# Performance work log

Hardware: AMD Instinct MI355X
Metric: run time of the kernel (lower is better)

The kernel has to match this reference:

```python
import jax, jax.numpy as jnp
import numpy as np

INV_L_MIN, INV_L_MAX = 0.5, 2.0

def _gelu(v):
    return jax.nn.gelu(v, approximate=False)  # torch F.gelu default = exact erf

def compute_gradient(f, directed_edges, edge_gradient_weights):
    # f: [b, c, n] ; directed_edges: [b, e, 2] (target, source) ; egw: [b, e, d]
    f = jnp.transpose(f, (0, 2, 1))                      # [b, n, c]
    b, n, c = f.shape
    e, d = edge_gradient_weights.shape[1], edge_gradient_weights.shape[2]
    target, source = directed_edges[..., 0], directed_edges[..., 1]
    fs = jnp.take_along_axis(f, source[:, :, None], axis=1)   # [b, e, c]
    ft = jnp.take_along_axis(f, target[:, :, None], axis=1)   # [b, e, c]
    # einsum('bed,bec->becd') then reshape -> channel-major (c*d) layout
    msg = (edge_gradient_weights[:, :, None, :] * (fs - ft)[:, :, :, None]).reshape(b, e, c * d)
    seg = (target + n * jnp.arange(b, dtype=target.dtype)[:, None]).reshape(-1)
    grad = jax.ops.segment_sum(msg.reshape(b * e, c * d), seg, num_segments=b * n)
    return jnp.transpose(grad.reshape(b, n, c * d), (0, 2, 1))  # [b, c*d, n]

def spectral_conv(x, wc, ws_, w0, bc, bs, b0, wbc, wbs, wb0):
    # x: [b, c, n]; bases: [b, n, k, w]; weights: [c, o, k, w]
    xc = jnp.einsum('bcx,bxkw->bckw', x, wbc)
    xs = jnp.einsum('bcx,bxkw->bckw', x, wbs)
    x0 = jnp.einsum('bcx,bxkw->bckw', x, wb0)
    fc = jnp.einsum('bckw,cokw->bokw', xc, wc) - jnp.einsum('bckw,cokw->bokw', xs, ws_)
    fs = jnp.einsum('bckw,cokw->bokw', xs, wc) + jnp.einsum('bckw,cokw->bokw', xc, ws_)
    f0 = jnp.einsum('bckw,cokw->bokw', x0, w0)
    return (jnp.einsum('bokw,bxkw->box', f0, b0)
            + 2 * jnp.einsum('bokw,bxkw->box', fc, bc)
            - 2 * jnp.einsum('bokw,bxkw->box', fs, bs))

def setup_inputs():
    key = jax.random.key(0)
    ks = jax.random.split(key, 16)
    B, N, E = 4, 20000, 100000
    NDIMS, NMEAS, NMODES = 3, 1, 32
    C, L = 128, 3
    IN_DIM, FC_DIM, OUT_DIM = 3, 128, 1
    f32 = jnp.float32
    inp = {}
    inp['x'] = jax.random.normal(ks[0], (B, N, IN_DIM), f32)
    inp['node_mask'] = jnp.ones((B, N, 1), jnp.int32)
    inp['nodes'] = jax.random.uniform(ks[1], (B, N, NDIMS), f32)
    inp['node_weights'] = jax.random.uniform(ks[2], (B, N, NMEAS), f32) / N
    inp['directed_edges'] = jax.random.randint(ks[3], (B, E, 2), 0, N, jnp.int32)
    inp['edge_gradient_weights'] = jax.random.normal(ks[4], (B, E, NDIMS), f32)
    # modes k = 2*pi*K/L0, K integer-like
    inp['modes'] = (2 * jnp.pi * jax.random.randint(ks[5], (NMODES, NDIMS, NMEAS), 1, 9)).astype(f32)
    # scaled_logit(1.0, 0.5, 2.0): sigmoid(l)=1/3 -> l=log(0.5)
    inp['inv_L_scale_latent'] = jnp.full((NDIMS, NMEAS), np.log(0.5), f32)
    inp['fc0_w'] = jax.random.normal(ks[6], (C, IN_DIM), f32) / np.sqrt(IN_DIM)
    inp['fc0_b'] = jnp.zeros((C,), f32)
    sc = 1.0 / (C * C)
    inp['swc'] = sc * jax.random.uniform(ks[7], (L, C, C, NMODES, NMEAS), f32)
    inp['sws'] = sc * jax.random.uniform(ks[8], (L, C, C, NMODES, NMEAS), f32)
    inp['sw0'] = sc * jax.random.uniform(ks[9], (L, C, C, 1, NMEAS), f32)
    inp['ww'] = jax.random.normal(ks[10], (L, C, C), f32) / np.sqrt(C)
    inp['wb'] = jnp.zeros((L, C), f32)
    inp['gw'] = jax.random.normal(ks[11], (L, C, NDIMS * C), f32) / np.sqrt(NDIMS * C)
    inp['gb'] = jnp.zeros((L, C), f32)
    inp['fc1_w'] = jax.random.normal(ks[12], (FC_DIM, C), f32) / np.sqrt(C)
    inp['fc1_b'] = jnp.zeros((FC_DIM,), f32)
    inp['fc2_w'] = jax.random.normal(ks[13], (OUT_DIM, FC_DIM), f32) / np.sqrt(FC_DIM)
    inp['fc2_b'] = jnp.zeros((OUT_DIM,), f32)
    return inp

def reference(x, node_mask, nodes, node_weights, directed_edges, edge_gradient_weights,
              modes, inv_L_scale_latent, fc0_w, fc0_b, swc, sws, sw0, ww, wb, gw, gb,
              fc1_w, fc1_b, fc2_w, fc2_b):
    inv_L = INV_L_MIN + (INV_L_MAX - INV_L_MIN) * jax.nn.sigmoid(inv_L_scale_latent)  # [d, w]
    t = jnp.einsum('bxd,kdw->bxkw', nodes, modes * inv_L[None])
    bc, bs = jnp.cos(t), jnp.sin(t)
    b0 = jnp.ones(t.shape[:2] + (1, t.shape[3]), t.dtype)
    w = node_weights[:, :, None, :]
    wbc, wbs, wb0 = bc * w, bs * w, b0 * w
    h = jnp.einsum('bni,ci->bnc', x, fc0_w) + fc0_b        # lift
    h = jnp.transpose(h, (0, 2, 1))                        # [b, C, n]
    L = swc.shape[0]
    for i in range(L):
        h1 = spectral_conv(h, swc[i], sws[i], sw0[i], bc, bs, b0, wbc, wbs, wb0)
        h2 = jnp.einsum('oc,bcn->bon', ww[i], h) + wb[i][None, :, None]
        g = compute_gradient(h, directed_edges, edge_gradient_weights)
        h3 = jnp.einsum('oc,bcn->bon', gw[i], g) + gb[i][None, :, None]
        h = h1 + h2 + h3
        if i != L - 1:
            h = _gelu(h)
    h = jnp.transpose(h, (0, 2, 1))                        # [b, n, C]
    h = _gelu(h @ fc1_w.T + fc1_b)
    return h @ fc2_w.T + fc2_b                             # [b, n, out_dim]
```

## Files before the change

kernel.cpp:

```cpp
#include <hip/hip_runtime.h>
#include <math.h>

#define B_ 4
#define N_ 20000
#define E_ 100000
#define C_ 128
#define K_ 32
#define NPAD 20480
#define NROWS (B_*N_ + 128)

typedef __attribute__((ext_vector_type(8))) short short8;
typedef __attribute__((ext_vector_type(4))) float floatx4;
typedef __attribute__((ext_vector_type(4))) unsigned int uintx4;
typedef __attribute__((ext_vector_type(2))) unsigned int uintx2;

__device__ __forceinline__ float gelu_exact(float x){
    return 0.5f * x * (1.0f + erff(x * 0.70710678118654752f));
}

__device__ __forceinline__ unsigned short f2bf(float f){
    unsigned int u = __builtin_bit_cast(unsigned int, f);
    u += 0x7FFFu + ((u >> 16) & 1u);
    return (unsigned short)(u >> 16);
}
__device__ __forceinline__ unsigned int pack2(float a, float b){
    return (unsigned int)f2bf(a) | ((unsigned int)f2bf(b) << 16);
}
__device__ __forceinline__ float bf2f(unsigned short u){
    unsigned int v = ((unsigned int)u) << 16;
    return __builtin_bit_cast(float, v);
}
__device__ __forceinline__ float u2f(unsigned int u){
    return __builtin_bit_cast(float, u);
}


__global__ __launch_bounds__(256) void basis_kernel(
    const float* __restrict__ nodes, const float* __restrict__ nw,
    const float* __restrict__ modes, const float* __restrict__ latent,
    unsigned short* __restrict__ bcb, unsigned short* __restrict__ bsb,
    unsigned short* __restrict__ wBt)
{
    __shared__ float lx[64], ly[64], lz[64], lwv[64];
    __shared__ unsigned short lTc[32*64], lTs[32*64];
    int b = blockIdx.y, n0 = blockIdx.x*64;
    int tid = threadIdx.x;
    size_t bN = (size_t)b*N_;
    if (tid < 64){
        int n = n0 + tid;
        float iL0 = 0.5f + 1.5f/(1.f+expf(-latent[0]));
        float iL1 = 0.5f + 1.5f/(1.f+expf(-latent[1]));
        float iL2 = 0.5f + 1.5f/(1.f+expf(-latent[2]));
        if (n < N_){
            lx[tid] = nodes[(bN+n)*3+0]*iL0;
            ly[tid] = nodes[(bN+n)*3+1]*iL1;
            lz[tid] = nodes[(bN+n)*3+2]*iL2;
            lwv[tid] = nw[bN+n];
        } else { lx[tid]=0.f; ly[tid]=0.f; lz[tid]=0.f; lwv[tid]=0.f; }
    }
    __syncthreads();
    int node = tid>>2, k0 = (tid&3)*8;
    float p0 = lx[node], p1 = ly[node], p2 = lz[node], w = lwv[node];
    float cv[8], sv[8];
    #pragma unroll
    for (int i=0;i<8;i++){
        int k = k0+i;
        float t = p0*modes[k*3+0] + p1*modes[k*3+1] + p2*modes[k*3+2];
        cv[i] = cosf(t); sv[i] = sinf(t);
        lTc[k*64 + node] = f2bf(w*cv[i]);
        lTs[k*64 + node] = f2bf(w*sv[i]);
    }
    int gn = n0 + node;
    if (gn < N_){
        uintx4 uc = (uintx4){pack2(cv[0],cv[1]), pack2(cv[2],cv[3]),
                             pack2(cv[4],cv[5]), pack2(cv[6],cv[7])};
        uintx4 us = (uintx4){pack2(sv[0],sv[1]), pack2(sv[2],sv[3]),
                             pack2(sv[4],sv[5]), pack2(sv[6],sv[7])};
        *(uintx4*)&bcb[(bN+gn)*K_ + k0] = uc;
        *(uintx4*)&bsb[(bN+gn)*K_ + k0] = us;
    }
    __syncthreads();
    #pragma unroll
    for (int i=0;i<5;i++){
        int idx = i*256 + tid;
        int row = idx>>4, seg = idx&15;
        unsigned short v0,v1,v2,v3;
        if (row < 32){
            v0=lTc[row*64+seg*4+0]; v1=lTc[row*64+seg*4+1];
            v2=lTc[row*64+seg*4+2]; v3=lTc[row*64+seg*4+3];
        } else if (row < 64){
            int r = row-32;
            v0=lTs[r*64+seg*4+0]; v1=lTs[r*64+seg*4+1];
            v2=lTs[r*64+seg*4+2]; v3=lTs[r*64+seg*4+3];
        } else if (row == 64){
            v0=f2bf(lwv[seg*4+0]); v1=f2bf(lwv[seg*4+1]);
            v2=f2bf(lwv[seg*4+2]); v3=f2bf(lwv[seg*4+3]);
        } else { v0=v1=v2=v3=0; }
        uintx2 u;
        u.x = (unsigned int)v0 | ((unsigned int)v1<<16);
        u.y = (unsigned int)v2 | ((unsigned int)v3<<16);
        *(uintx2*)&wBt[((size_t)b*80+row)*NPAD + n0 + seg*4] = u;
    }
}


__global__ __launch_bounds__(256) void fc0_kernel(
    const float* __restrict__ x, const float* __restrict__ w,
    const float* __restrict__ bvec, unsigned short* __restrict__ hN,
    unsigned short* __restrict__ hT)
{
    int idx = blockIdx.x*256 + threadIdx.x;
    if (idx >= B_*N_) return;
    int b = idx / N_, n = idx - b*N_;
    float x0 = x[(size_t)idx*3+0], x1 = x[(size_t)idx*3+1], x2 = x[(size_t)idx*3+2];
    unsigned short* hr = hN + (size_t)idx*C_;
    for (int c=0;c<C_;c+=4){
        float4 v;
        v.x = bvec[c+0] + x0*w[(c+0)*3] + x1*w[(c+0)*3+1] + x2*w[(c+0)*3+2];
        v.y = bvec[c+1] + x0*w[(c+1)*3] + x1*w[(c+1)*3+1] + x2*w[(c+1)*3+2];
        v.z = bvec[c+2] + x0*w[(c+2)*3] + x1*w[(c+2)*3+1] + x2*w[(c+2)*3+2];
        v.w = bvec[c+3] + x0*w[(c+3)*3] + x1*w[(c+3)*3+1] + x2*w[(c+3)*3+2];
        uintx2 u; u.x = pack2(v.x,v.y); u.y = pack2(v.z,v.w);
        *(uintx2*)(hr+c) = u;
        hT[((size_t)b*C_+c+0)*NPAD + n] = f2bf(v.x);
        hT[((size_t)b*C_+c+1)*NPAD + n] = f2bf(v.y);
        hT[((size_t)b*C_+c+2)*NPAD + n] = f2bf(v.z);
        hT[((size_t)b*C_+c+3)*NPAD + n] = f2bf(v.w);
    }
}


__global__ __launch_bounds__(256) void hist_kernel(
    const int* __restrict__ edges, int* __restrict__ cnt)
{
    int idx = blockIdx.x*256 + threadIdx.x;
    if (idx >= B_*E_) return;
    int b = idx / E_;
    int t = edges[(size_t)idx*2];
    atomicAdd(cnt + b*N_ + t, 1);
}

__global__ __launch_bounds__(1024) void scan_kernel(
    const int* __restrict__ cnt, int* __restrict__ rowptr, int* __restrict__ cur)
{
    __shared__ int wsum[16];
    int b = blockIdx.x, tid = threadIdx.x;
    int lane = tid & 63, wv = tid >> 6;
    const int CHUNK = 20;
    int start = tid * CHUNK;
    int lc[CHUNK];
    int lsum = 0;
    #pragma unroll
    for (int i=0;i<CHUNK;i++){
        int n = start + i;
        int v = (n < N_) ? cnt[b*N_+n] : 0;
        lc[i] = v; lsum += v;
    }
    int v = lsum;
    #pragma unroll
    for (int off=1; off<64; off<<=1){
        int t = __shfl_up(v, off, 64);
        if (lane >= off) v += t;
    }
    if (lane == 63) wsum[wv] = v;
    __syncthreads();
    if (wv == 0 && lane < 16){
        int wv2 = wsum[lane];
        #pragma unroll
        for (int off=1; off<16; off<<=1){
            int t = __shfl_up(wv2, off, 64);
            if (lane >= off) wv2 += t;
        }
        wsum[lane] = wv2;
    }
    __syncthreads();
    int waveoff = (wv == 0) ? 0 : wsum[wv-1];
    int excl = waveoff + v - lsum;
    #pragma unroll
    for (int i=0;i<CHUNK;i++){
        int n = start + i;
        if (n < N_){
            rowptr[b*(N_+1)+n] = excl;
            cur[b*N_+n] = excl;
            excl += lc[i];
        }
    }
    if (tid == 0) rowptr[b*(N_+1)+N_] = E_;
}

__global__ __launch_bounds__(256) void fill_kernel(
    const int* __restrict__ edges, const float* __restrict__ egw,
    int* __restrict__ cur, uintx4* __restrict__ epack)
{
    int idx = blockIdx.x*256 + threadIdx.x;
    if (idx >= B_*E_) return;
    int b = idx / E_;
    int t = edges[(size_t)idx*2];
    int src = edges[(size_t)idx*2+1];
    uintx4 rec;
    rec.x = (unsigned int)src;
    rec.y = __builtin_bit_cast(unsigned int, egw[(size_t)idx*3+0]);
    rec.z = __builtin_bit_cast(unsigned int, egw[(size_t)idx*3+1]);
    rec.w = __builtin_bit_cast(unsigned int, egw[(size_t)idx*3+2]);
    int pos = atomicAdd(cur + b*N_ + t, 1);
    epack[(size_t)b*E_ + pos] = rec;
}


__global__ __launch_bounds__(256) void wconv_kernel(
    const float* __restrict__ ww, const float* __restrict__ gw,
    unsigned short* __restrict__ wcat3)
{
    int o = blockIdx.x, l = blockIdx.y, t = threadIdx.x;
    const float* ww_l = ww + (size_t)l*C_*C_;
    const float* gw_l = gw + (size_t)l*C_*C_*3;
    int k = t*2;
    float a, bv;
    if (k < 128){ a = ww_l[(size_t)o*C_ + k];      bv = ww_l[(size_t)o*C_ + k + 1]; }
    else        { a = gw_l[(size_t)o*384 + k-128]; bv = gw_l[(size_t)o*384 + k-127]; }
    *(unsigned int*)&wcat3[((size_t)l*C_ + o)*512 + k] = pack2(a, bv);
}

__global__ __launch_bounds__(64) void fc1conv_kernel(
    const float* __restrict__ fc1w, unsigned short* __restrict__ w16)
{
    int o = blockIdx.x, t = threadIdx.x;
    int k = t*2;
    *(unsigned int*)&w16[(size_t)o*C_ + k] = pack2(fc1w[(size_t)o*C_+k], fc1w[(size_t)o*C_+k+1]);
}


__global__ __launch_bounds__(256) void stageA_kernel(
    const unsigned short* __restrict__ hT, const unsigned short* __restrict__ wBt,
    float* __restrict__ part)
{
    __shared__ unsigned short As[80*72];
    __shared__ unsigned short Bs[128*72];
    int b = blockIdx.y, blk = blockIdx.x;
    int tid = threadIdx.x;
    int wv = tid>>6, lane = tid&63, l15 = lane&15, quad = lane>>4;
    floatx4 acc[5][2];
    #pragma unroll
    for (int mt=0;mt<5;mt++){ acc[mt][0]=(floatx4){0,0,0,0}; acc[mt][1]=(floatx4){0,0,0,0}; }
    size_t hbase = (size_t)b*C_*NPAD;
    size_t wbase = (size_t)b*80*NPAD;
    for (int cidx=0; cidx<5; ++cidx){
        int n0c = blk*320 + cidx*64;
        #pragma unroll
        for (int i=0;i<3;i++){
            int idx = i*256 + tid;
            if (idx < 640){
                int row = idx>>3, seg = idx&7;
                uintx4 v = *(const uintx4*)&wBt[wbase + (size_t)row*NPAD + n0c + seg*8];
                *(uintx4*)&As[row*72 + seg*8] = v;
            }
        }
        #pragma unroll
        for (int i=0;i<4;i++){
            int idx = i*256 + tid;
            int row = idx>>3, seg = idx&7;
            int node = n0c + seg*8;
            uintx4 v = (uintx4){0,0,0,0};
            if (node < N_)
                v = *(const uintx4*)&hT[hbase + (size_t)row*NPAD + node];
            *(uintx4*)&Bs[row*72 + seg*8] = v;
        }
        __syncthreads();
        #pragma unroll
        for (int ks=0; ks<2; ks++){
            short8 bfrag[2];
            #pragma unroll
            for (int ot=0;ot<2;ot++)
                bfrag[ot] = *(const short8*)&Bs[(wv*32+ot*16+l15)*72 + ks*32 + quad*8];
            #pragma unroll
            for (int mt=0;mt<5;mt++){
                short8 af = *(const short8*)&As[(mt*16+l15)*72 + ks*32 + quad*8];
                acc[mt][0] = __builtin_amdgcn_mfma_f32_16x16x32_bf16(af, bfrag[0], acc[mt][0], 0,0,0);
                acc[mt][1] = __builtin_amdgcn_mfma_f32_16x16x32_bf16(af, bfrag[1], acc[mt][1], 0,0,0);
            }
        }
        __syncthreads();
    }
    float* pblk = part + ((size_t)(b*64+blk))*80*C_;
    #pragma unroll
    for (int mt=0;mt<5;mt++){
        #pragma unroll
        for (int ot=0;ot<2;ot++){
            int c = wv*32 + ot*16 + l15;
            #pragma unroll
            for (int r=0;r<4;r++){
                int kcol = mt*16 + quad*4 + r;
                pblk[kcol*C_ + c] = acc[mt][ot][r];
            }
        }
    }
}

__global__ __launch_bounds__(256) void reducePart_kernel(
    const float* __restrict__ part, float* __restrict__ xq)
{
    int idx = blockIdx.x*256 + threadIdx.x;
    if (idx >= B_*80*C_) return;
    int b = idx / (80*C_);
    int r = idx - b*80*C_;
    float s = 0.f;
    for (int blk=0; blk<64; blk++)
        s += part[((size_t)(b*64+blk))*80*C_ + r];
    xq[idx] = s;
}


__global__ __launch_bounds__(256) void mix_kernel(
    const float* __restrict__ xq, const float* __restrict__ swc_l,
    const float* __restrict__ sws_l, const float* __restrict__ sw0_l,
    unsigned short* __restrict__ wfb, float* __restrict__ f0)
{
    __shared__ float s64[4][64];
    int o = blockIdx.x, tid = threadIdx.x;
    int b = tid >> 6, t = tid & 63;
    int k = t & 31; bool isS = t >= 32;
    const float* xqb = xq + (size_t)b*80*C_;
    float acc = 0.f;
    for (int c=0;c<C_;c++){
        float xc = xqb[k*C_ + c], xs = xqb[(32+k)*C_ + c];
        float wc = swc_l[((size_t)c*C_+o)*K_ + k];
        float ws = sws_l[((size_t)c*C_+o)*K_ + k];
        acc += isS ? (xs*wc + xc*ws) : (xc*wc - xs*ws);
    }
    wfb[((size_t)b*C_+o)*64 + t] = f2bf(isS ? -2.f*acc : 2.f*acc);
    float p = xqb[64*C_ + t]      * sw0_l[(size_t)t*C_+o]
            + xqb[64*C_ + 64 + t] * sw0_l[(size_t)(t+64)*C_+o];
    s64[b][t] = p; __syncthreads();
    if (t==0){
        float s=0.f;
        for (int i=0;i<64;i++) s += s64[b][i];
        f0[b*C_+o] = s;
    }
}


__global__ __launch_bounds__(256) void grad_kernel(
    const unsigned short* __restrict__ hN, const uintx4* __restrict__ epack,
    const int* __restrict__ rowptr, unsigned short* __restrict__ g)
{
    int flat = blockIdx.x;
    int xcd = flat & 7;
    int b = xcd >> 1;
    int grp = (flat >> 3)*2 + (xcd & 1);
    int n = grp*4 + (threadIdx.x >> 6);
    int cp = threadIdx.x & 63;
    size_t bN = (size_t)b*N_;
    size_t bE = (size_t)b*E_;
    int r0 = rowptr[b*(N_+1)+n], r1 = rowptr[b*(N_+1)+n+1];
    unsigned int hcu = *(const unsigned int*)&hN[(bN+n)*C_ + cp*2];
    float hc0 = bf2f((unsigned short)hcu), hc1 = bf2f((unsigned short)(hcu>>16));
    float a00=0.f,a01=0.f,a02=0.f, a10=0.f,a11=0.f,a12=0.f;
    int i = r0;
    for (; i + 1 < r1; i += 2){
        uintx4 p0 = epack[bE + i];
        uintx4 p1 = epack[bE + i + 1];
        int s0 = (int)p0.x, s1 = (int)p1.x;
        unsigned int u0 = *(const unsigned int*)&hN[(bN+s0)*C_ + cp*2];
        unsigned int u1 = *(const unsigned int*)&hN[(bN+s1)*C_ + cp*2];
        float w00 = u2f(p0.y), w01 = u2f(p0.z), w02 = u2f(p0.w);
        float w10 = u2f(p1.y), w11 = u2f(p1.z), w12 = u2f(p1.w);
        float d00 = bf2f((unsigned short)u0) - hc0;
        float d01 = bf2f((unsigned short)(u0>>16)) - hc1;
        float d10 = bf2f((unsigned short)u1) - hc0;
        float d11 = bf2f((unsigned short)(u1>>16)) - hc1;
        a00 += w00*d00; a01 += w01*d00; a02 += w02*d00;
        a10 += w00*d01; a11 += w01*d01; a12 += w02*d01;
        a00 += w10*d10; a01 += w11*d10; a02 += w12*d10;
        a10 += w10*d11; a11 += w11*d11; a12 += w12*d11;
    }
    if (i < r1){
        uintx4 p0 = epack[bE + i];
        int s0 = (int)p0.x;
        unsigned int u0 = *(const unsigned int*)&hN[(bN+s0)*C_ + cp*2];
        float w00 = u2f(p0.y), w01 = u2f(p0.z), w02 = u2f(p0.w);
        float d00 = bf2f((unsigned short)u0) - hc0;
        float d01 = bf2f((unsigned short)(u0>>16)) - hc1;
        a00 += w00*d00; a01 += w01*d00; a02 += w02*d00;
        a10 += w00*d01; a11 += w01*d01; a12 += w02*d01;
    }
    unsigned short* gr = g + (bN+n)*(size_t)384 + cp*6;
    *(unsigned int*)(gr+0) = pack2(a00,a01);
    *(unsigned int*)(gr+2) = pack2(a02,a10);
    *(unsigned int*)(gr+4) = pack2(a11,a12);
}


__global__ __launch_bounds__(256) void gemm_kernel(
    const unsigned short* __restrict__ hN, const unsigned short* __restrict__ g,
    const unsigned short* __restrict__ bcb, const unsigned short* __restrict__ bsb,
    const unsigned short* __restrict__ wcat, const unsigned short* __restrict__ wfb,
    const float* __restrict__ wb_l, const float* __restrict__ gb_l,
    const float* __restrict__ f0,
    unsigned short* __restrict__ hNo, unsigned short* __restrict__ hT, int apply_gelu)
{
    __shared__ unsigned short As[2][64*72];
    int b = blockIdx.y;
    int nb0 = blockIdx.x*64;
    int tid = threadIdx.x;
    int a_n = tid>>2, a_s = tid&3;
    int wv = tid>>6, lane = tid&63, l15 = lane&15, quad = lane>>4;
    floatx4 acc[4][2];
    #pragma unroll
    for (int mt=0;mt<4;mt++)
        #pragma unroll
        for (int ot=0;ot<2;ot++) acc[mt][ot] = (floatx4){0.f,0.f,0.f,0.f};
    size_t bN = (size_t)b*N_;
    int gn = nb0 + a_n; bool av = gn < N_;
    size_t row = bN + (size_t)(av ? gn : 0);
    const unsigned short* hrow  = hN + row*C_;
    const unsigned short* grow  = g  + row*384;
    const unsigned short* bcrow = bcb + row*K_;
    const unsigned short* bsrow = bsb + row*K_;
    int o0 = wv*32 + l15, o1 = o0 + 16;
    const unsigned short* w0p = wcat + (size_t)o0*512 + quad*8;
    const unsigned short* w1p = wcat + (size_t)o1*512 + quad*8;
    const unsigned short* fb0 = wfb + ((size_t)b*C_ + o0)*64 + quad*8;
    const unsigned short* fb1 = wfb + ((size_t)b*C_ + o1)*64 + quad*8;

    auto loadA = [&](int ch, uintx4& v0, uintx4& v1){
        v0 = (uintx4){0,0,0,0}; v1 = (uintx4){0,0,0,0};
        if (av){
            if (ch < 8){
                const uintx4* p = (ch<2) ? (const uintx4*)(hrow + ch*64 + a_s*16)
                                         : (const uintx4*)(grow + (ch-2)*64 + a_s*16);
                v0 = p[0]; v1 = p[1];
            } else {
                const uintx4* p = (a_s < 2) ? (const uintx4*)(bcrow + a_s*16)
                                            : (const uintx4*)(bsrow + (a_s-2)*16);
                v0 = p[0]; v1 = p[1];
            }
        }
    };

    uintx4 c0, c1;
    loadA(0, c0, c1);
    *(uintx4*)&As[0][a_n*72 + a_s*16]     = c0;
    *(uintx4*)&As[0][a_n*72 + a_s*16 + 8] = c1;
    int p = 0;
    for (int ch=0; ch<9; ++ch){
        uintx4 n0v, n1v;
        if (ch < 8) loadA(ch+1, n0v, n1v);
        __syncthreads();
        #pragma unroll
        for (int ks=0; ks<2; ks++){
            short8 bfr0, bfr1;
            if (ch < 8){
                bfr0 = *(const short8*)(w0p + ch*64 + ks*32);
                bfr1 = *(const short8*)(w1p + ch*64 + ks*32);
            } else {
                bfr0 = *(const short8*)(fb0 + ks*32);
                bfr1 = *(const short8*)(fb1 + ks*32);
            }
            #pragma unroll
            for (int mt=0; mt<4; mt++){
                short8 af = *(const short8*)&As[p][(mt*16+l15)*72 + ks*32 + quad*8];
                acc[mt][0] = __builtin_amdgcn_mfma_f32_16x16x32_bf16(af, bfr0, acc[mt][0], 0,0,0);
                acc[mt][1] = __builtin_amdgcn_mfma_f32_16x16x32_bf16(af, bfr1, acc[mt][1], 0,0,0);
            }
        }
        if (ch < 8){
            *(uintx4*)&As[1-p][a_n*72 + a_s*16]     = n0v;
            *(uintx4*)&As[1-p][a_n*72 + a_s*16 + 8] = n1v;
            p ^= 1;
        }
    }
    float biasv[2]; int oo[2];
    oo[0]=o0; oo[1]=o1;
    #pragma unroll
    for (int ot=0;ot<2;ot++)
        biasv[ot] = wb_l[oo[ot]] + gb_l[oo[ot]] + f0[(size_t)b*C_ + oo[ot]];
    unsigned short* AsF = &As[0][0];
    if (apply_gelu) __syncthreads();
    #pragma unroll
    for (int mt=0;mt<4;mt++){
        #pragma unroll
        for (int ot=0;ot<2;ot++){
            int nb = nb0 + mt*16 + quad*4;
            float v4[4];
            #pragma unroll
            for (int r=0;r<4;r++){
                float vv = acc[mt][ot][r] + biasv[ot];
                if (apply_gelu) vv = gelu_exact(vv);
                v4[r] = vv;
                if (nb + r < N_) hNo[(bN+nb+r)*C_ + oo[ot]] = f2bf(vv);
            }
            if (apply_gelu){
                uintx2 u; u.x = pack2(v4[0],v4[1]); u.y = pack2(v4[2],v4[3]);
                *(uintx2*)&AsF[oo[ot]*72 + mt*16 + quad*4] = u;
            }
        }
    }
    if (apply_gelu){
        __syncthreads();
        int orow = tid>>1, half = tid&1;
        uintx4 u0 = *(const uintx4*)&AsF[orow*72 + half*32];
        uintx4 u1 = *(const uintx4*)&AsF[orow*72 + half*32 + 8];
        unsigned short* dst = &hT[((size_t)b*C_ + orow)*NPAD + nb0 + half*32];
        *(uintx4*)dst       = u0;
        *(uintx4*)(dst + 8) = u1;
    }
}


__global__ __launch_bounds__(256) void final_kernel(
    const unsigned short* __restrict__ hN, const unsigned short* __restrict__ fc1b16,
    const float* __restrict__ fc1b, const float* __restrict__ fc2w,
    const float* __restrict__ fc2b, float* __restrict__ out)
{
    __shared__ unsigned short As[64*72];
    __shared__ float pp[4*64];
    int b = blockIdx.y;
    int nb0 = blockIdx.x*64;
    int tid = threadIdx.x;
    int a_n = tid>>2, a_s = tid&3;
    int wv = tid>>6, lane = tid&63, l15 = lane&15, quad = lane>>4;
    floatx4 acc[4][2];
    #pragma unroll
    for (int mt=0;mt<4;mt++){ acc[mt][0]=(floatx4){0,0,0,0}; acc[mt][1]=(floatx4){0,0,0,0}; }
    size_t bN = (size_t)b*N_;
    int gn = nb0 + a_n; bool av = gn < N_;
    size_t row = bN + (size_t)(av ? gn : 0);
    const unsigned short* hrow = hN + row*C_;
    int o0 = wv*32 + l15, o1 = o0 + 16;
    const unsigned short* w0p = fc1b16 + (size_t)o0*C_ + quad*8;
    const unsigned short* w1p = fc1b16 + (size_t)o1*C_ + quad*8;

    for (int ch=0; ch<2; ++ch){
        uintx4 v0 = (uintx4){0,0,0,0}, v1 = (uintx4){0,0,0,0};
        if (av){
            const uintx4* pptr = (const uintx4*)(hrow + ch*64 + a_s*16);
            v0 = pptr[0]; v1 = pptr[1];
        }
        *(uintx4*)&As[a_n*72 + a_s*16]     = v0;
        *(uintx4*)&As[a_n*72 + a_s*16 + 8] = v1;
        __syncthreads();
        #pragma unroll
        for (int ks=0; ks<2; ks++){
            short8 bfr0 = *(const short8*)(w0p + ch*64 + ks*32);
            short8 bfr1 = *(const short8*)(w1p + ch*64 + ks*32);
            #pragma unroll
            for (int mt=0; mt<4; mt++){
                short8 af = *(const short8*)&As[(mt*16+l15)*72 + ks*32 + quad*8];
                acc[mt][0] = __builtin_amdgcn_mfma_f32_16x16x32_bf16(af, bfr0, acc[mt][0], 0,0,0);
                acc[mt][1] = __builtin_amdgcn_mfma_f32_16x16x32_bf16(af, bfr1, acc[mt][1], 0,0,0);
            }
        }
        __syncthreads();
    }
    float fw0 = fc2w[o0], fw1 = fc2w[o1];
    float b0 = fc1b[o0], b1 = fc1b[o1];
    #pragma unroll
    for (int mt=0;mt<4;mt++){
        float s[4];
        #pragma unroll
        for (int r=0;r<4;r++)
            s[r] = fw0*gelu_exact(acc[mt][0][r] + b0) + fw1*gelu_exact(acc[mt][1][r] + b1);
        #pragma unroll
        for (int m=1;m<16;m<<=1)
            #pragma unroll
            for (int r=0;r<4;r++)
                s[r] += __shfl_xor(s[r], m, 16);
        if (l15 < 4){
            float v = (l15==0)?s[0]:(l15==1)?s[1]:(l15==2)?s[2]:s[3];
            pp[wv*64 + mt*16 + quad*4 + l15] = v;
        }
    }
    __syncthreads();
    if (tid < 64){
        float sum = pp[tid] + pp[64+tid] + pp[128+tid] + pp[192+tid] + fc2b[0];
        int n = nb0 + tid;
        if (n < N_) out[bN + n] = sum;
    }
}


extern "C" void kernel_launch(void* const* d_in, const int* in_sizes, int n_in,
                              void* d_out, int out_size, void* d_ws, size_t ws_size,
                              hipStream_t stream)
{
    const float* x      = (const float*)d_in[0];
    const float* nodes  = (const float*)d_in[2];
    const float* nw     = (const float*)d_in[3];
    const int*   edges  = (const int*)  d_in[4];
    const float* egw    = (const float*)d_in[5];
    const float* modes  = (const float*)d_in[6];
    const float* latent = (const float*)d_in[7];
    const float* fc0w   = (const float*)d_in[8];
    const float* fc0b   = (const float*)d_in[9];
    const float* swc    = (const float*)d_in[10];
    const float* sws    = (const float*)d_in[11];
    const float* sw0    = (const float*)d_in[12];
    const float* ww     = (const float*)d_in[13];
    const float* wb     = (const float*)d_in[14];
    const float* gw     = (const float*)d_in[15];
    const float* gb     = (const float*)d_in[16];
    const float* fc1w   = (const float*)d_in[17];
    const float* fc1b   = (const float*)d_in[18];
    const float* fc2w   = (const float*)d_in[19];
    const float* fc2b   = (const float*)d_in[20];
    float* out = (float*)d_out;

    char* W = (char*)d_ws;
    size_t off = 0;
    unsigned short* bcB = (unsigned short*)(W+off); off += (size_t)NROWS*K_*2;
    unsigned short* bsB = (unsigned short*)(W+off); off += (size_t)NROWS*K_*2;
    unsigned short* wBt = (unsigned short*)(W+off); off += (size_t)B_*80*NPAD*2;
    unsigned short* hT  = (unsigned short*)(W+off); off += (size_t)B_*C_*NPAD*2;
    unsigned short* hNa = (unsigned short*)(W+off); off += (size_t)NROWS*C_*2;
    unsigned short* hNb = (unsigned short*)(W+off); off += (size_t)NROWS*C_*2;
    unsigned short* g   = (unsigned short*)(W+off); off += (size_t)NROWS*C_*3*2;
    unsigned short* wcat3=(unsigned short*)(W+off); off += (size_t)3*C_*512*2;
    unsigned short* wfb = (unsigned short*)(W+off); off += (size_t)B_*C_*64*2;
    unsigned short* fcw16=(unsigned short*)(W+off); off += (size_t)C_*C_*2;
    float* part = (float*)(W+off); off += (size_t)B_*64*80*C_*4;
    float* xq   = (float*)(W+off); off += (size_t)B_*80*C_*4;
    float* f0   = (float*)(W+off); off += (size_t)B_*C_*4;
    off = (off + 15) & ~(size_t)15;
    uintx4* epack = (uintx4*)(W+off); off += (size_t)B_*E_*16;
    int* cnt    = (int*)(W+off); off += (size_t)B_*N_*4;
    int* rowptr = (int*)(W+off); off += (size_t)B_*(N_+1)*4 + 16;
    int* cur    = (int*)(W+off); off += (size_t)B_*N_*4;

    (void)hipMemsetAsync(cnt, 0, (size_t)B_*N_*sizeof(int), stream);
    basis_kernel<<<dim3(NPAD/64, B_), 256, 0, stream>>>(
        nodes, nw, modes, latent, bcB, bsB, wBt);
    fc0_kernel  <<<(B_*N_+255)/256, 256, 0, stream>>>(x, fc0w, fc0b, hNa, hT);
    hist_kernel <<<(B_*E_+255)/256, 256, 0, stream>>>(edges, cnt);
    scan_kernel <<<B_, 1024, 0, stream>>>(cnt, rowptr, cur);
    fill_kernel <<<(B_*E_+255)/256, 256, 0, stream>>>(edges, egw, cur, epack);
    wconv_kernel<<<dim3(C_,3), 256, 0, stream>>>(ww, gw, wcat3);
    fc1conv_kernel<<<C_, 64, 0, stream>>>(fc1w, fcw16);

    unsigned short* hc = hNa; unsigned short* hn = hNb;
    for (int l=0; l<3; ++l){
        stageA_kernel<<<dim3(64,B_), 256, 0, stream>>>(hT, wBt, part);
        reducePart_kernel<<<(B_*80*C_+255)/256, 256, 0, stream>>>(part, xq);
        mix_kernel<<<C_, 256, 0, stream>>>(
            xq, swc + (size_t)l*C_*C_*K_, sws + (size_t)l*C_*C_*K_,
            sw0 + (size_t)l*C_*C_, wfb, f0);
        grad_kernel<<<N_, 256, 0, stream>>>(hc, epack, rowptr, g);
        gemm_kernel<<<dim3((N_+63)/64,B_), 256, 0, stream>>>(
            hc, g, bcB, bsB, wcat3 + (size_t)l*C_*512, wfb,
            wb + (size_t)l*C_, gb + (size_t)l*C_,
            f0, hn, hT, (l<2) ? 1 : 0);
        unsigned short* t = hc; hc = hn; hn = t;
    }
    final_kernel<<<dim3((N_+63)/64,B_), 256, 0, stream>>>(
        hc, fcw16, fc1b, fc2w, fc2b, out);
}
```

Before: 569.7 us.

## Pipeline GEMM A-tiles via direct global-to-LDS loads with a four-stage ring

In gemm_kernel, the register-staged, double-buffered shared-memory load of the A operand is replaced by asynchronous global_load_lds transfers into a four-slot LDS ring. The tile layout changes from padded rows to an XOR-swizzled layout so fragment reads avoid bank conflicts. Weight B fragments are preloaded into a three-deep register ring, and hand-placed vmcnt waits plus barriers order the stages. The aim is to hide global-load latency behind MFMA work and drop the VGPR round-trip for A. In exchange, the per-row bounds check is gone, so the last block reads past N into adjacent or padded rows, and the hand-counted waits are fragile.

```diff
diff --git a/kernel.cpp b/kernel.cpp
--- a/kernel.cpp
+++ b/kernel.cpp
@@ -390,6 +390,9 @@
 }
 
 
+#define WAITV(n) asm volatile("s_waitcnt vmcnt(" #n ")" ::: "memory")
+#define BAR() __builtin_amdgcn_s_barrier()
+
 __global__ __launch_bounds__(256) void gemm_kernel(
     const unsigned short* __restrict__ hN, const unsigned short* __restrict__ g,
     const unsigned short* __restrict__ bcb, const unsigned short* __restrict__ bsb,
@@ -398,11 +401,10 @@
     const float* __restrict__ f0,
     unsigned short* __restrict__ hNo, unsigned short* __restrict__ hT, int apply_gelu)
 {
-    __shared__ unsigned short As[2][64*72];
+    __shared__ unsigned short As4[4][4096];
     int b = blockIdx.y;
     int nb0 = blockIdx.x*64;
     int tid = threadIdx.x;
-    int a_n = tid>>2, a_s = tid&3;
     int wv = tid>>6, lane = tid&63, l15 = lane&15, quad = lane>>4;
     floatx4 acc[4][2];
     #pragma unroll
@@ -410,71 +412,80 @@
         #pragma unroll
         for (int ot=0;ot<2;ot++) acc[mt][ot] = (floatx4){0.f,0.f,0.f,0.f};
     size_t bN = (size_t)b*N_;
-    int gn = nb0 + a_n; bool av = gn < N_;
-    size_t row = bN + (size_t)(av ? gn : 0);
-    const unsigned short* hrow  = hN + row*C_;
-    const unsigned short* grow  = g  + row*384;
-    const unsigned short* bcrow = bcb + row*K_;
-    const unsigned short* bsrow = bsb + row*K_;
+
+    const unsigned short* sh[2]; const unsigned short* sg[2]; const unsigned short* sb[2];
+    #pragma unroll
+    for (int q=0;q<2;q++){
+        int li = q*256 + tid;
+        int row = li>>3, col = (li&7) ^ (row&7);
+        size_t gr = bN + (size_t)(nb0 + row);
+        sh[q] = hN + gr*C_  + col*8;
+        sg[q] = g  + gr*384 + col*8;
+        sb[q] = (col < 4) ? (bcb + gr*K_ + col*8) : (bsb + gr*K_ + (col-4)*8);
+    }
     int o0 = wv*32 + l15, o1 = o0 + 16;
     const unsigned short* w0p = wcat + (size_t)o0*512 + quad*8;
     const unsigned short* w1p = wcat + (size_t)o1*512 + quad*8;
     const unsigned short* fb0 = wfb + ((size_t)b*C_ + o0)*64 + quad*8;
     const unsigned short* fb1 = wfb + ((size_t)b*C_ + o1)*64 + quad*8;
 
-    auto loadA = [&](int ch, uintx4& v0, uintx4& v1){
-        v0 = (uintx4){0,0,0,0}; v1 = (uintx4){0,0,0,0};
-        if (av){
-            if (ch < 8){
-                const uintx4* p = (ch<2) ? (const uintx4*)(hrow + ch*64 + a_s*16)
-                                         : (const uintx4*)(grow + (ch-2)*64 + a_s*16);
-                v0 = p[0]; v1 = p[1];
-            } else {
-                const uintx4* p = (a_s < 2) ? (const uintx4*)(bcrow + a_s*16)
-                                            : (const uintx4*)(bsrow + (a_s-2)*16);
-                v0 = p[0]; v1 = p[1];
-            }
-        }
-    };
-
-    uintx4 c0, c1;
-    loadA(0, c0, c1);
-    *(uintx4*)&As[0][a_n*72 + a_s*16]     = c0;
-    *(uintx4*)&As[0][a_n*72 + a_s*16 + 8] = c1;
-    int p = 0;
-    for (int ch=0; ch<9; ++ch){
-        uintx4 n0v, n1v;
-        if (ch < 8) loadA(ch+1, n0v, n1v);
-        __syncthreads();
-        #pragma unroll
-        for (int ks=0; ks<2; ks++){
-            short8 bfr0, bfr1;
-            if (ch < 8){
-                bfr0 = *(const short8*)(w0p + ch*64 + ks*32);
-                bfr1 = *(const short8*)(w1p + ch*64 + ks*32);
-            } else {
-                bfr0 = *(const short8*)(fb0 + ks*32);
-                bfr1 = *(const short8*)(fb1 + ks*32);
-            }
-            #pragma unroll
-            for (int mt=0; mt<4; mt++){
-                short8 af = *(const short8*)&As[p][(mt*16+l15)*72 + ks*32 + quad*8];
-                acc[mt][0] = __builtin_amdgcn_mfma_f32_16x16x32_bf16(af, bfr0, acc[mt][0], 0,0,0);
-                acc[mt][1] = __builtin_amdgcn_mfma_f32_16x16x32_bf16(af, bfr1, acc[mt][1], 0,0,0);
-            }
-        }
-        if (ch < 8){
-            *(uintx4*)&As[1-p][a_n*72 + a_s*16]     = n0v;
-            *(uintx4*)&As[1-p][a_n*72 + a_s*16 + 8] = n1v;
-            p ^= 1;
-        }
-    }
+    short8 bb[3][2][2];
+
+#define LOADB(ch) do{ \
+    if ((ch) < 8){ \
+        bb[(ch)%3][0][0] = *(const short8*)(w0p + (ch)*64); \
+        bb[(ch)%3][0][1] = *(const short8*)(w0p + (ch)*64 + 32); \
+        bb[(ch)%3][1][0] = *(const short8*)(w1p + (ch)*64); \
+        bb[(ch)%3][1][1] = *(const short8*)(w1p + (ch)*64 + 32); \
+    } else { \
+        bb[(ch)%3][0][0] = *(const short8*)(fb0); \
+        bb[(ch)%3][0][1] = *(const short8*)(fb0 + 32); \
+        bb[(ch)%3][1][0] = *(const short8*)(fb1); \
+        bb[(ch)%3][1][1] = *(const short8*)(fb1 + 32); \
+    } }while(0)
+
+#define STAGE1(ch,q) \
+    __builtin_amdgcn_global_load_lds( \
+        (const __attribute__((address_space(1))) void*)( \
+            ((ch) < 2) ? (sh[q] + (ch)*64) : \
+            ((ch) < 8) ? (sg[q] + ((ch)-2)*64) : sb[q] ), \
+        (__attribute__((address_space(3))) void*)&As4[(ch)&3][(q)*2048 + wv*512], \
+        16, 0, 0)
+#define STAGE(ch) do{ STAGE1(ch,0); STAGE1(ch,1); }while(0)
+
+#define COMPUTE(ch) do{ \
+    _Pragma("unroll") \
+    for (int ks=0; ks<2; ks++){ \
+        _Pragma("unroll") \
+        for (int mt=0; mt<4; mt++){ \
+            short8 af = *(const short8*)&As4[(ch)&3][(mt*16+l15)*64 + (((ks*4+quad)^(l15&7))*8)]; \
+            acc[mt][0] = __builtin_amdgcn_mfma_f32_16x16x32_bf16(af, bb[(ch)%3][0][ks], acc[mt][0], 0,0,0); \
+            acc[mt][1] = __builtin_amdgcn_mfma_f32_16x16x32_bf16(af, bb[(ch)%3][1][ks], acc[mt][1], 0,0,0); \
+        } } }while(0)
+
+    LOADB(0); LOADB(1);
+    STAGE(0); STAGE(1); STAGE(2);
+    WAITV(4); BAR(); LOADB(2); STAGE(3); COMPUTE(0);
+    WAITV(8); BAR(); LOADB(3); STAGE(4); COMPUTE(1);
+    WAITV(8); BAR(); LOADB(4); STAGE(5); COMPUTE(2);
+    WAITV(8); BAR(); LOADB(5); STAGE(6); COMPUTE(3);
+    WAITV(8); BAR(); LOADB(6); STAGE(7); COMPUTE(4);
+    WAITV(8); BAR(); LOADB(7); STAGE(8); COMPUTE(5);
+    WAITV(8); BAR(); LOADB(8);           COMPUTE(6);
+    WAITV(6); BAR();                     COMPUTE(7);
+    WAITV(0); BAR();                     COMPUTE(8);
+
+#undef LOADB
+#undef STAGE1
+#undef STAGE
+#undef COMPUTE
+
     float biasv[2]; int oo[2];
     oo[0]=o0; oo[1]=o1;
     #pragma unroll
     for (int ot=0;ot<2;ot++)
         biasv[ot] = wb_l[oo[ot]] + gb_l[oo[ot]] + f0[(size_t)b*C_ + oo[ot]];
-    unsigned short* AsF = &As[0][0];
+    unsigned short* AsF = &As4[0][0];
     if (apply_gelu) __syncthreads();
     #pragma unroll
     for (int mt=0;mt<4;mt++){
```

After: 548.6 us. 3.7% less time.
